# Performance work log

Hardware: AMD Instinct MI355X
Metric: run time of the kernel (lower is better)

Reference implementation:

```python
import jax, jax.numpy as jnp
import numpy as np

TOP_K = 2  # moe_top_k


def setup_inputs() -> dict:
    key = jax.random.key(0)
    k0, k1, k2, k3 = jax.random.split(key, 4)
    SL, BS, H, F, E = 2048, 4, 1024, 1024, 8
    x = jax.random.normal(k0, (SL, BS, H), dtype=jnp.float32)
    w_router = jax.random.normal(k1, (H, E), dtype=jnp.float32) * 0.02
    w1 = jax.random.normal(k2, (E, H, F), dtype=jnp.float32) * 0.02  # per-expert map weights
    w2 = jax.random.normal(k3, (E, F, H), dtype=jnp.float32) * 0.02  # per-expert reduce weights
    return {"x": x, "w_router": w_router, "w1": w1, "w2": w2}


def reference(x, w_router, w1, w2):
    # dMoA forward: router -> dropless dispatch -> per-expert map GEMM ->
    # per-expert reduce GEMM -> expert-weighted combine. Dropless = no capacity
    # dropping, so a dense all-experts compute + per-token selection is exactly
    # equivalent in math to the sort/gather/grouped-GEMM/scatter pipeline.
    sl, bs, h = x.shape
    E = w1.shape[0]
    xt = x.reshape(-1, h)  # [T, H], T = sl*bs
    T = xt.shape[0]

    # LearnedRouter: softmax over expert logits, then top-k weights/indices
    scores = jax.nn.softmax(xt @ w_router, axis=-1)       # [T, E]
    expert_weights, top_experts = jax.lax.top_k(scores, TOP_K)  # [T, K]

    # load-balancing loss (router.loss): E * sum_e f_e * p_e
    onehot = jax.nn.one_hot(top_experts, E, dtype=xt.dtype)  # [T, K, E]
    tokens_frac = onehot.sum(axis=(0, 1)) / (T * TOP_K)      # f_e
    probs_mean = scores.mean(axis=0)                         # p_e
    loss = E * jnp.sum(tokens_frac * probs_mean)

    # map: per-expert linear H->F, select the top-k experts' outputs per token
    y_all = jnp.einsum('th,ehf->tef', xt, w1)                 # [T, E, F]
    h_tk = jnp.take_along_axis(y_all, top_experts[:, :, None], axis=1)  # [T, K, F]

    # reduce: weighted scatter-combine, then per-expert linear F->H
    hw = jnp.einsum('tke,tk,tkf->tef', onehot, expert_weights, h_tk)  # [T, E, F]
    out = jnp.einsum('tef,efh->th', hw, w2)                   # [T, H]
    return out.reshape(sl, bs, h), loss
```

## Files before the change

### kernel.cpp

```cpp
#include <hip/hip_runtime.h>
#include <hip/hip_bf16.h>
#include <stdint.h>


#define HD 1024
#define FD 1024
#define EN 8

typedef __attribute__((ext_vector_type(8))) short bf16x8;
typedef __attribute__((ext_vector_type(4))) float f32x4;

__device__ __forceinline__ void gload16(const void* g, void* l) {
    __builtin_amdgcn_global_load_lds(
        (const __attribute__((address_space(1))) unsigned int*)g,
        (__attribute__((address_space(3))) unsigned int*)l, 16, 0, 0);
}

__device__ __forceinline__ ushort f2bf(float v) {
    __hip_bfloat16 h = __float2bfloat16(v);
    return *(ushort*)&h;
}
__device__ __forceinline__ float bf2f(ushort u) {
    unsigned int w = ((unsigned int)u) << 16;
    float f; __builtin_memcpy(&f, &w, 4); return f;
}

__global__ __launch_bounds__(256) void router_kernel(
    const float* __restrict__ x, const float* __restrict__ wrt,
    ushort* __restrict__ xb,
    int* __restrict__ top_e, float* __restrict__ top_w,
    int* __restrict__ counts, float* __restrict__ probsum)
{
    __shared__ int   cnt_s[EN];
    __shared__ float ps_s[EN];
    int tid = threadIdx.x;
    if (tid < EN) { cnt_s[tid] = 0; ps_s[tid] = 0.f; }
    __syncthreads();

    int wid = tid >> 6, lane = tid & 63;
    int t = blockIdx.x * 4 + wid;
    const float4* xr4 = (const float4*)(x + (size_t)t * HD);
    ushort4* xbo = (ushort4*)(xb + (size_t)t * HD);
    float acc[EN];
#pragma unroll
    for (int e = 0; e < EN; e++) acc[e] = 0.f;
#pragma unroll
    for (int it = 0; it < 4; it++) {
        float4 xv = xr4[it * 64 + lane];
        ushort4 o; o.x = f2bf(xv.x); o.y = f2bf(xv.y); o.z = f2bf(xv.z); o.w = f2bf(xv.w);
        xbo[it * 64 + lane] = o;
        int h0 = it * 256 + lane * 4;
        float xs[4] = {xv.x, xv.y, xv.z, xv.w};
#pragma unroll
        for (int j = 0; j < 4; j++) {
            const float4* wp = (const float4*)(wrt + (size_t)(h0 + j) * EN);
            float4 wa = wp[0], wb = wp[1];
            acc[0] += xs[j] * wa.x; acc[1] += xs[j] * wa.y;
            acc[2] += xs[j] * wa.z; acc[3] += xs[j] * wa.w;
            acc[4] += xs[j] * wb.x; acc[5] += xs[j] * wb.y;
            acc[6] += xs[j] * wb.z; acc[7] += xs[j] * wb.w;
        }
    }
#pragma unroll
    for (int off = 32; off >= 1; off >>= 1) {
#pragma unroll
        for (int e = 0; e < EN; e++) acc[e] += __shfl_xor(acc[e], off, 64);
    }
    if (lane == 0) {
        float m = acc[0];
#pragma unroll
        for (int e = 1; e < EN; e++) m = fmaxf(m, acc[e]);
        float p[EN], s = 0.f;
#pragma unroll
        for (int e = 0; e < EN; e++) { p[e] = expf(acc[e] - m); s += p[e]; }
        float inv = 1.f / s;
#pragma unroll
        for (int e = 0; e < EN; e++) p[e] *= inv;
        int e0 = 0;
#pragma unroll
        for (int e = 1; e < EN; e++) if (p[e] > p[e0]) e0 = e;
        int e1 = (e0 == 0) ? 1 : 0;
#pragma unroll
        for (int e = 0; e < EN; e++) {
            if (e == e0) continue;
            if (p[e] > p[e1]) e1 = e;
        }
        top_e[t * 2] = e0;  top_e[t * 2 + 1] = e1;
        top_w[t * 2] = p[e0]; top_w[t * 2 + 1] = p[e1];
        atomicAdd(&cnt_s[e0], 1); atomicAdd(&cnt_s[e1], 1);
#pragma unroll
        for (int e = 0; e < EN; e++) atomicAdd(&ps_s[e], p[e]);
    }
    __syncthreads();
    if (tid < EN) {
        atomicAdd(&counts[tid], cnt_s[tid]);
        atomicAdd(&probsum[tid], ps_s[tid]);
    }
}

__global__ void prep_kernel(const int* __restrict__ counts,
                            const float* __restrict__ probsum,
                            int* __restrict__ offs, float* __restrict__ loss_out)
{
    int off = 0; float loss = 0.f;
    for (int e = 0; e < EN; e++) {
        offs[e] = off;
        off += counts[e];
        loss += ((float)counts[e] / 16384.f) * (probsum[e] / 8192.f);
    }
    offs[EN] = off;
    *loss_out = 8.f * loss;
}

__global__ __launch_bounds__(256) void dispatch_kernel(
    const int* __restrict__ top_e, const float* __restrict__ top_w,
    const int* __restrict__ offs, int* __restrict__ cursor,
    int* __restrict__ tok_list, float* __restrict__ w_list)
{
    int t = blockIdx.x * 256 + threadIdx.x;
    int lane = threadIdx.x & 63;
#pragma unroll
    for (int k = 0; k < 2; k++) {
        int e = top_e[t * 2 + k];
        int idx = 0;
#pragma unroll
        for (int ex = 0; ex < EN; ex++) {
            unsigned long long m = __ballot(e == ex);
            if (e == ex) {
                int cnt = __popcll(m);
                int leader = __ffsll(m) - 1;
                int pos = 0;
                if (lane == leader) pos = atomicAdd(&cursor[ex * 16], cnt);
                pos = __shfl(pos, leader, 64);
                int rank = __popcll(m & ((1ull << lane) - 1ull));
                idx = offs[ex] + pos + rank;
            }
        }
        tok_list[idx] = t * 2 + k;
        w_list[idx] = top_w[t * 2 + k];
    }
}

__global__ __launch_bounds__(256) void transpose_conv_kernel(
    const float* __restrict__ w1, const float* __restrict__ w2,
    ushort* __restrict__ w1b, ushort* __restrict__ w2b)
{
    __shared__ float tile[32][33];
    int bid = blockIdx.x;
    const float* in; ushort* outp;
    if (bid >= 8192) { in = w2; outp = w2b; bid -= 8192; }
    else             { in = w1; outp = w1b; }
    int e  = bid >> 10;
    int t2 = bid & 1023;
    int tb = t2 >> 5;
    int ta = t2 & 31;
    const float* pin = in + ((size_t)e << 20);
    ushort* pout = outp + ((size_t)e << 20);
    int tx = threadIdx.x & 31, ty = threadIdx.x >> 5;
#pragma unroll
    for (int j = 0; j < 4; j++)
        tile[ty + j * 8][tx] = pin[(size_t)(ta * 32 + ty + j * 8) * 1024 + tb * 32 + tx];
    __syncthreads();
#pragma unroll
    for (int j = 0; j < 4; j++)
        pout[(size_t)(tb * 32 + ty + j * 8) * 1024 + ta * 32 + tx] =
            f2bf(tile[tx][ty + j * 8]);
}


__global__ __launch_bounds__(256) void map_gemm(
    const ushort* __restrict__ xb, const ushort* __restrict__ w1b,
    ushort* __restrict__ hbuf,
    const int* __restrict__ tok_list, const float* __restrict__ w_list,
    const int* __restrict__ offs)
{
    __shared__ __align__(16) short lA[128][64];
    __shared__ __align__(16) short lB[128][64];
    __shared__ int   tok_s[128];
    __shared__ float wt_s[128];

    int g = blockIdx.x;
    int e = g & 7, q = g >> 3, nb = q & 7, rb = q >> 3;
    int base = offs[e], cnt = offs[e + 1] - base;
    int row0 = rb << 7;
    if (row0 >= cnt) return;
    int rem = cnt - row0;
    int tid = threadIdx.x;
    if (tid < 128) {
        int r = row0 + tid; if (r > cnt - 1) r = cnt - 1;
        tok_s[tid] = tok_list[base + r];
        wt_s[tid]  = w_list[base + r];
    }
    __syncthreads();

    int lane = tid & 63, w = tid >> 6;
    int wm = w >> 1, wn = w & 1;
    int lo = lane & 15, hi = lane >> 4, rx = lane & 7;

    int lr = lane >> 3;
    int kseg = ((lane & 7) ^ lr) << 3;
    const ushort* pA[4]; const ushort* pB[4];
    const ushort* wbase = w1b + ((size_t)e << 20);
#pragma unroll
    for (int i = 0; i < 4; i++) {
        int rowT = w * 32 + i * 8 + lr;
        pA[i] = xb + (size_t)(tok_s[rowT] >> 1) * HD + kseg;
        pB[i] = wbase + (size_t)(nb * 128 + rowT) * HD + kseg;
    }

    f32x4 acc[4][4];
#pragma unroll
    for (int m = 0; m < 4; m++)
#pragma unroll
        for (int n = 0; n < 4; n++) acc[m][n] = (f32x4){0.f, 0.f, 0.f, 0.f};

    for (int kt = 0; kt < 16; ++kt) {
#pragma unroll
        for (int i = 0; i < 4; i++) {
            int rowT = w * 32 + i * 8 + lr;
            gload16(pA[i], &lA[rowT][0]);
            gload16(pB[i], &lB[rowT][0]);
            pA[i] += 64; pB[i] += 64;
        }
        __syncthreads();
        bf16x8 af[4][2], bg[4][2];
#pragma unroll
        for (int m = 0; m < 4; m++)
#pragma unroll
            for (int ks = 0; ks < 2; ks++)
                af[m][ks] = *(const bf16x8*)&lA[wm * 64 + m * 16 + lo][((ks * 4 + hi) ^ rx) << 3];
#pragma unroll
        for (int n = 0; n < 4; n++)
#pragma unroll
            for (int ks = 0; ks < 2; ks++)
                bg[n][ks] = *(const bf16x8*)&lB[wn * 64 + n * 16 + lo][((ks * 4 + hi) ^ rx) << 3];
#pragma unroll
        for (int ks = 0; ks < 2; ks++)
#pragma unroll
            for (int m = 0; m < 4; m++)
#pragma unroll
                for (int n = 0; n < 4; n++)
                    acc[m][n] = __builtin_amdgcn_mfma_f32_16x16x32_bf16(af[m][ks], bg[n][ks], acc[m][n], 0, 0, 0);
        __syncthreads();
    }

    short* ep = ((short*)lA) + w * 4096;
#pragma unroll
    for (int m = 0; m < 4; m++)
#pragma unroll
        for (int r = 0; r < 4; r++) {
            int row_l = m * 16 + hi * 4 + r;
            int rswz = (row_l & 7) << 4;
            float wgt = wt_s[wm * 64 + row_l];
#pragma unroll
            for (int n = 0; n < 4; n++) {
                int colb = (n * 16 + lo) * 2;
                ep[(row_l * 128 + (colb ^ rswz)) >> 1] = f2bf(acc[m][n][r] * wgt);
            }
        }
    __syncthreads();
    size_t outbase = (size_t)(base + row0);
    int colg0 = (nb << 7) + wn * 64;
#pragma unroll
    for (int j = 0; j < 8; j++) {
        int row_l = j * 8 + (lane >> 3);
        int r_blk = wm * 64 + row_l;
        int sb = ((lane & 7) * 16) ^ ((row_l & 7) << 4);
        bf16x8 v = *(const bf16x8*)&ep[(row_l * 128 + sb) >> 1];
        if (r_blk < rem)
            *(bf16x8*)&hbuf[(outbase + r_blk) * FD + colg0 + (lane & 7) * 8] = v;
    }
}

__global__ __launch_bounds__(256) void reduce_gemm(
    const ushort* __restrict__ hbuf, const ushort* __restrict__ w2b,
    ushort* __restrict__ obuf,
    const int* __restrict__ tok_list, const int* __restrict__ offs)
{
    __shared__ __align__(16) short lA[128][64];
    __shared__ __align__(16) short lB[128][64];
    __shared__ int tok_s[128];

    int g = blockIdx.x;
    int e = g & 7, q = g >> 3, nb = q & 7, rb = q >> 3;
    int base = offs[e], cnt = offs[e + 1] - base;
    int row0 = rb << 7;
    if (row0 >= cnt) return;
    int rem = cnt - row0;
    int tid = threadIdx.x;
    if (tid < 128) {
        int r = row0 + tid; if (r > cnt - 1) r = cnt - 1;
        tok_s[tid] = tok_list[base + r];
    }
    __syncthreads();

    int lane = tid & 63, w = tid >> 6;
    int wm = w >> 1, wn = w & 1;
    int lo = lane & 15, hi = lane >> 4, rx = lane & 7;

    int lr = lane >> 3;
    int kseg = ((lane & 7) ^ lr) << 3;
    const ushort* pA[4]; const ushort* pB[4];
    const ushort* wbase = w2b + ((size_t)e << 20);
#pragma unroll
    for (int i = 0; i < 4; i++) {
        int rowT = w * 32 + i * 8 + lr;
        int ar = row0 + rowT; if (ar > cnt - 1) ar = cnt - 1;
        pA[i] = hbuf + (size_t)(base + ar) * FD + kseg;
        pB[i] = wbase + (size_t)(nb * 128 + rowT) * FD + kseg;
    }

    f32x4 acc[4][4];
#pragma unroll
    for (int m = 0; m < 4; m++)
#pragma unroll
        for (int n = 0; n < 4; n++) acc[m][n] = (f32x4){0.f, 0.f, 0.f, 0.f};

    for (int kt = 0; kt < 16; ++kt) {
#pragma unroll
        for (int i = 0; i < 4; i++) {
            int rowT = w * 32 + i * 8 + lr;
            gload16(pA[i], &lA[rowT][0]);
            gload16(pB[i], &lB[rowT][0]);
            pA[i] += 64; pB[i] += 64;
        }
        __syncthreads();
        bf16x8 af[4][2], bg[4][2];
#pragma unroll
        for (int m = 0; m < 4; m++)
#pragma unroll
            for (int ks = 0; ks < 2; ks++)
                af[m][ks] = *(const bf16x8*)&lA[wm * 64 + m * 16 + lo][((ks * 4 + hi) ^ rx) << 3];
#pragma unroll
        for (int n = 0; n < 4; n++)
#pragma unroll
            for (int ks = 0; ks < 2; ks++)
                bg[n][ks] = *(const bf16x8*)&lB[wn * 64 + n * 16 + lo][((ks * 4 + hi) ^ rx) << 3];
#pragma unroll
        for (int ks = 0; ks < 2; ks++)
#pragma unroll
            for (int m = 0; m < 4; m++)
#pragma unroll
                for (int n = 0; n < 4; n++)
                    acc[m][n] = __builtin_amdgcn_mfma_f32_16x16x32_bf16(af[m][ks], bg[n][ks], acc[m][n], 0, 0, 0);
        __syncthreads();
    }

    short* ep = ((short*)lA) + w * 4096;
#pragma unroll
    for (int m = 0; m < 4; m++)
#pragma unroll
        for (int r = 0; r < 4; r++) {
            int row_l = m * 16 + hi * 4 + r;
            int rswz = (row_l & 7) << 4;
#pragma unroll
            for (int n = 0; n < 4; n++) {
                int colb = (n * 16 + lo) * 2;
                ep[(row_l * 128 + (colb ^ rswz)) >> 1] = f2bf(acc[m][n][r]);
            }
        }
    __syncthreads();
    int colg0 = (nb << 7) + wn * 64;
#pragma unroll
    for (int j = 0; j < 8; j++) {
        int row_l = j * 8 + (lane >> 3);
        int r_blk = wm * 64 + row_l;
        int sb = ((lane & 7) * 16) ^ ((row_l & 7) << 4);
        bf16x8 v = *(const bf16x8*)&ep[(row_l * 128 + sb) >> 1];
        if (r_blk < rem)
            *(bf16x8*)&obuf[(size_t)tok_s[r_blk] * HD + colg0 + (lane & 7) * 8] = v;
    }
}

__global__ __launch_bounds__(256) void combine_kernel(
    const ushort* __restrict__ obuf, float* __restrict__ out)
{
    int g = blockIdx.x * 256 + threadIdx.x;
    int t = g >> 7, c8 = (g & 127) << 3;
    const ushort* p = obuf + (size_t)t * 2048 + c8;
    bf16x8 a = *(const bf16x8*)p;
    bf16x8 b = *(const bf16x8*)(p + 1024);
    float o[8];
#pragma unroll
    for (int i = 0; i < 8; i++)
        o[i] = bf2f((ushort)a[i]) + bf2f((ushort)b[i]);
    float* q = out + (size_t)t * HD + c8;
    *(float4*)q       = (float4){o[0], o[1], o[2], o[3]};
    *(float4*)(q + 4) = (float4){o[4], o[5], o[6], o[7]};
}

extern "C" void kernel_launch(void* const* d_in, const int* in_sizes, int n_in,
                              void* d_out, int out_size, void* d_ws, size_t ws_size,
                              hipStream_t stream)
{
    const float* x   = (const float*)d_in[0];
    const float* wrt = (const float*)d_in[1];
    const float* w1  = (const float*)d_in[2];
    const float* w2  = (const float*)d_in[3];
    float* out = (float*)d_out;

    uint8_t* ws = (uint8_t*)d_ws;
    ushort* xb   = (ushort*)(ws);
    ushort* w1b  = (ushort*)(ws + (16u << 20));
    ushort* obuf = (ushort*)(ws);
    ushort* w2b  = (ushort*)(ws + (32u << 20));
    ushort* hbuf = (ushort*)(ws + (48u << 20));
    uint8_t* p80 = ws + (80u << 20);
    int*   tok_list = (int*)(p80);
    float* w_list   = (float*)(p80 + (64u << 10));
    int*   top_e    = (int*)(p80 + (128u << 10));
    float* top_w    = (float*)(p80 + (192u << 10));
    uint8_t* ctr    = p80 + (256u << 10);
    int*   counts   = (int*)(ctr);
    float* probsum  = (float*)(ctr + 64);
    int*   offs     = (int*)(ctr + 128);
    int*   cursor   = (int*)(ctr + 256);
    float* loss_out = out + 8388608;

    hipMemsetAsync(ctr, 0, 1024, stream);

    router_kernel<<<2048, 256, 0, stream>>>(x, wrt, xb, top_e, top_w, counts, probsum);
    prep_kernel<<<1, 1, 0, stream>>>(counts, probsum, offs, loss_out);
    dispatch_kernel<<<32, 256, 0, stream>>>(top_e, top_w, offs, cursor, tok_list, w_list);
    transpose_conv_kernel<<<16384, 256, 0, stream>>>(w1, w2, w1b, w2b);
    map_gemm<<<1152, 256, 0, stream>>>(xb, w1b, hbuf, tok_list, w_list, offs);
    reduce_gemm<<<1152, 256, 0, stream>>>(hbuf, w2b, obuf, tok_list, offs);
    combine_kernel<<<4096, 256, 0, stream>>>(obuf, out);
}
```

Measured before the change: 205.6 us.

## Fuse router with weight transpose, fold prep into dispatch, widen GEMM N-tile

Merges the router and weight transpose/convert into one launch. The transpose now uses 64x32 tiles with float4 loads and 16-byte bf16 stores. The single-thread prep kernel is folded into dispatch, where every thread recomputes the expert offsets from counts. Both expert GEMMs move from 128x128 to 128x256 output tiles, which halves the grid and reuses each A tile across twice as many columns, at the cost of more accumulator registers and LDS per block.

```diff
diff --git a/kernel.cpp b/kernel.cpp
--- a/kernel.cpp
+++ b/kernel.cpp
@@ -25,20 +25,53 @@
     float f; __builtin_memcpy(&f, &w, 4); return f;
 }
 
-__global__ __launch_bounds__(256) void router_kernel(
+__global__ __launch_bounds__(256) void fused_rt_kernel(
     const float* __restrict__ x, const float* __restrict__ wrt,
-    ushort* __restrict__ xb,
+    const float* __restrict__ w1, const float* __restrict__ w2,
+    ushort* __restrict__ xb, ushort* __restrict__ w1b, ushort* __restrict__ w2b,
     int* __restrict__ top_e, float* __restrict__ top_w,
     int* __restrict__ counts, float* __restrict__ probsum)
 {
+    __shared__ float smem[64 * 33];
+    int bid = blockIdx.x;
+    int tid = threadIdx.x;
+
+    if (bid < 8192) {
+        const float* in; ushort* outp;
+        if (bid >= 4096) { in = w2; outp = w2b; bid -= 4096; }
+        else             { in = w1; outp = w1b; }
+        int e  = bid >> 9;
+        int t2 = bid & 511;
+        int kt = t2 >> 5;
+        int nt = t2 & 31;
+        const float* pin = in + ((size_t)e << 20) + (size_t)(kt * 64) * 1024 + nt * 32;
+        ushort* pout = outp + ((size_t)e << 20) + (size_t)(nt * 32) * 1024 + kt * 64;
+#pragma unroll
+        for (int s = 0; s < 2; s++) {
+            int slot = s * 256 + tid;
+            int kk = slot >> 3, c4 = slot & 7;
+            float4 v = *(const float4*)(pin + (size_t)kk * 1024 + c4 * 4);
+            float* d = &smem[kk * 33 + c4 * 4];
+            d[0] = v.x; d[1] = v.y; d[2] = v.z; d[3] = v.w;
+        }
+        __syncthreads();
+        {
+            int n = tid >> 3, ks = (tid & 7) * 8;
+            ushort us[8];
+#pragma unroll
+            for (int i = 0; i < 8; i++) us[i] = f2bf(smem[(ks + i) * 33 + n]);
+            *(uint4*)(pout + (size_t)n * 1024 + ks) = *(uint4*)us;
+        }
+        return;
+    }
+
     __shared__ int   cnt_s[EN];
     __shared__ float ps_s[EN];
-    int tid = threadIdx.x;
     if (tid < EN) { cnt_s[tid] = 0; ps_s[tid] = 0.f; }
     __syncthreads();
 
     int wid = tid >> 6, lane = tid & 63;
-    int t = blockIdx.x * 4 + wid;
+    int t = (bid - 8192) * 4 + wid;
     const float4* xr4 = (const float4*)(x + (size_t)t * HD);
     ushort4* xbo = (ushort4*)(xb + (size_t)t * HD);
     float acc[EN];
@@ -98,25 +131,26 @@
     }
 }
 
-__global__ void prep_kernel(const int* __restrict__ counts,
-                            const float* __restrict__ probsum,
-                            int* __restrict__ offs, float* __restrict__ loss_out)
-{
-    int off = 0; float loss = 0.f;
-    for (int e = 0; e < EN; e++) {
-        offs[e] = off;
-        off += counts[e];
-        loss += ((float)counts[e] / 16384.f) * (probsum[e] / 8192.f);
-    }
-    offs[EN] = off;
-    *loss_out = 8.f * loss;
-}
-
 __global__ __launch_bounds__(256) void dispatch_kernel(
+    const int* __restrict__ counts, const float* __restrict__ probsum,
     const int* __restrict__ top_e, const float* __restrict__ top_w,
-    const int* __restrict__ offs, int* __restrict__ cursor,
-    int* __restrict__ tok_list, float* __restrict__ w_list)
-{
+    int* __restrict__ cursor, int* __restrict__ tok_list,
+    float* __restrict__ w_list, int* __restrict__ offs_g,
+    float* __restrict__ loss_out)
+{
+    int offs[EN + 1]; offs[0] = 0;
+#pragma unroll
+    for (int e = 0; e < EN; e++) offs[e + 1] = offs[e] + counts[e];
+    if (blockIdx.x == 0 && threadIdx.x == 0) {
+        float loss = 0.f;
+#pragma unroll
+        for (int e = 0; e < EN; e++) {
+            offs_g[e] = offs[e];
+            loss += ((float)counts[e] / 16384.f) * (probsum[e] / 8192.f);
+        }
+        offs_g[EN] = offs[EN];
+        *loss_out = 8.f * loss;
+    }
     int t = blockIdx.x * 256 + threadIdx.x;
     int lane = threadIdx.x & 63;
 #pragma unroll
@@ -141,32 +175,6 @@
     }
 }
 
-__global__ __launch_bounds__(256) void transpose_conv_kernel(
-    const float* __restrict__ w1, const float* __restrict__ w2,
-    ushort* __restrict__ w1b, ushort* __restrict__ w2b)
-{
-    __shared__ float tile[32][33];
-    int bid = blockIdx.x;
-    const float* in; ushort* outp;
-    if (bid >= 8192) { in = w2; outp = w2b; bid -= 8192; }
-    else             { in = w1; outp = w1b; }
-    int e  = bid >> 10;
-    int t2 = bid & 1023;
-    int tb = t2 >> 5;
-    int ta = t2 & 31;
-    const float* pin = in + ((size_t)e << 20);
-    ushort* pout = outp + ((size_t)e << 20);
-    int tx = threadIdx.x & 31, ty = threadIdx.x >> 5;
-#pragma unroll
-    for (int j = 0; j < 4; j++)
-        tile[ty + j * 8][tx] = pin[(size_t)(ta * 32 + ty + j * 8) * 1024 + tb * 32 + tx];
-    __syncthreads();
-#pragma unroll
-    for (int j = 0; j < 4; j++)
-        pout[(size_t)(tb * 32 + ty + j * 8) * 1024 + ta * 32 + tx] =
-            f2bf(tile[tx][ty + j * 8]);
-}
-
 
 __global__ __launch_bounds__(256) void map_gemm(
     const ushort* __restrict__ xb, const ushort* __restrict__ w1b,
@@ -174,13 +182,14 @@
     const int* __restrict__ tok_list, const float* __restrict__ w_list,
     const int* __restrict__ offs)
 {
-    __shared__ __align__(16) short lA[128][64];
-    __shared__ __align__(16) short lB[128][64];
+    __shared__ __align__(16) short LS[(128 + 256) * 64];
     __shared__ int   tok_s[128];
     __shared__ float wt_s[128];
+    short (*lA)[64] = (short(*)[64])LS;
+    short (*lB)[64] = (short(*)[64])(LS + 128 * 64);
 
     int g = blockIdx.x;
-    int e = g & 7, q = g >> 3, nb = q & 7, rb = q >> 3;
+    int e = g & 7, q = g >> 3, nb = q & 3, rb = q >> 2;
     int base = offs[e], cnt = offs[e + 1] - base;
     int row0 = rb << 7;
     if (row0 >= cnt) return;
@@ -199,29 +208,29 @@
 
     int lr = lane >> 3;
     int kseg = ((lane & 7) ^ lr) << 3;
-    const ushort* pA[4]; const ushort* pB[4];
+    const ushort* pA[4];
     const ushort* wbase = w1b + ((size_t)e << 20);
 #pragma unroll
-    for (int i = 0; i < 4; i++) {
-        int rowT = w * 32 + i * 8 + lr;
-        pA[i] = xb + (size_t)(tok_s[rowT] >> 1) * HD + kseg;
-        pB[i] = wbase + (size_t)(nb * 128 + rowT) * HD + kseg;
-    }
-
-    f32x4 acc[4][4];
+    for (int i = 0; i < 4; i++)
+        pA[i] = xb + (size_t)(tok_s[w * 32 + i * 8 + lr] >> 1) * HD + kseg;
+    const ushort* pB0 = wbase + (size_t)(nb * 256 + w * 64 + lr) * HD + kseg;
+
+    f32x4 acc[4][8];
 #pragma unroll
     for (int m = 0; m < 4; m++)
 #pragma unroll
-        for (int n = 0; n < 4; n++) acc[m][n] = (f32x4){0.f, 0.f, 0.f, 0.f};
+        for (int n = 0; n < 8; n++) acc[m][n] = (f32x4){0.f, 0.f, 0.f, 0.f};
 
     for (int kt = 0; kt < 16; ++kt) {
 #pragma unroll
         for (int i = 0; i < 4; i++) {
-            int rowT = w * 32 + i * 8 + lr;
-            gload16(pA[i], &lA[rowT][0]);
-            gload16(pB[i], &lB[rowT][0]);
-            pA[i] += 64; pB[i] += 64;
-        }
+            gload16(pA[i], &lA[w * 32 + i * 8][0]);
+            pA[i] += 64;
+        }
+#pragma unroll
+        for (int i = 0; i < 8; i++)
+            gload16(pB0 + (size_t)i * 8 * HD, &lB[w * 64 + i * 8][0]);
+        pB0 += 64;
         __syncthreads();
         bf16x8 af[4][2], bg[4][2];
 #pragma unroll
@@ -233,7 +242,7 @@
         for (int n = 0; n < 4; n++)
 #pragma unroll
             for (int ks = 0; ks < 2; ks++)
-                bg[n][ks] = *(const bf16x8*)&lB[wn * 64 + n * 16 + lo][((ks * 4 + hi) ^ rx) << 3];
+                bg[n][ks] = *(const bf16x8*)&lB[wn * 128 + n * 16 + lo][((ks * 4 + hi) ^ rx) << 3];
 #pragma unroll
         for (int ks = 0; ks < 2; ks++)
 #pragma unroll
@@ -241,34 +250,50 @@
 #pragma unroll
                 for (int n = 0; n < 4; n++)
                     acc[m][n] = __builtin_amdgcn_mfma_f32_16x16x32_bf16(af[m][ks], bg[n][ks], acc[m][n], 0, 0, 0);
-        __syncthreads();
-    }
-
-    short* ep = ((short*)lA) + w * 4096;
-#pragma unroll
-    for (int m = 0; m < 4; m++)
-#pragma unroll
-        for (int r = 0; r < 4; r++) {
-            int row_l = m * 16 + hi * 4 + r;
-            int rswz = (row_l & 7) << 4;
-            float wgt = wt_s[wm * 64 + row_l];
-#pragma unroll
-            for (int n = 0; n < 4; n++) {
-                int colb = (n * 16 + lo) * 2;
-                ep[(row_l * 128 + (colb ^ rswz)) >> 1] = f2bf(acc[m][n][r] * wgt);
+#pragma unroll
+        for (int n = 0; n < 4; n++)
+#pragma unroll
+            for (int ks = 0; ks < 2; ks++)
+                bg[n][ks] = *(const bf16x8*)&lB[wn * 128 + 64 + n * 16 + lo][((ks * 4 + hi) ^ rx) << 3];
+#pragma unroll
+        for (int ks = 0; ks < 2; ks++)
+#pragma unroll
+            for (int m = 0; m < 4; m++)
+#pragma unroll
+                for (int n = 0; n < 4; n++)
+                    acc[m][n + 4] = __builtin_amdgcn_mfma_f32_16x16x32_bf16(af[m][ks], bg[n][ks], acc[m][n + 4], 0, 0, 0);
+        __syncthreads();
+    }
+
+    short* ep = LS + w * 4096;
+    size_t outbase = (size_t)(base + row0);
+#pragma unroll
+    for (int half = 0; half < 2; half++) {
+#pragma unroll
+        for (int m = 0; m < 4; m++)
+#pragma unroll
+            for (int r = 0; r < 4; r++) {
+                int row_l = m * 16 + hi * 4 + r;
+                int rswz = (row_l & 7) << 4;
+                float wgt = wt_s[wm * 64 + row_l];
+#pragma unroll
+                for (int n = 0; n < 4; n++) {
+                    int colb = (n * 16 + lo) * 2;
+                    ep[(row_l * 128 + (colb ^ rswz)) >> 1] = f2bf(acc[m][half * 4 + n][r] * wgt);
+                }
             }
-        }
-    __syncthreads();
-    size_t outbase = (size_t)(base + row0);
-    int colg0 = (nb << 7) + wn * 64;
-#pragma unroll
-    for (int j = 0; j < 8; j++) {
-        int row_l = j * 8 + (lane >> 3);
-        int r_blk = wm * 64 + row_l;
-        int sb = ((lane & 7) * 16) ^ ((row_l & 7) << 4);
-        bf16x8 v = *(const bf16x8*)&ep[(row_l * 128 + sb) >> 1];
-        if (r_blk < rem)
-            *(bf16x8*)&hbuf[(outbase + r_blk) * FD + colg0 + (lane & 7) * 8] = v;
+        __syncthreads();
+        int colg0 = (nb << 8) + wn * 128 + half * 64;
+#pragma unroll
+        for (int j = 0; j < 8; j++) {
+            int row_l = j * 8 + (lane >> 3);
+            int r_blk = wm * 64 + row_l;
+            int sb = ((lane & 7) * 16) ^ ((row_l & 7) << 4);
+            bf16x8 v = *(const bf16x8*)&ep[(row_l * 128 + sb) >> 1];
+            if (r_blk < rem)
+                *(bf16x8*)&hbuf[(outbase + r_blk) * FD + colg0 + (lane & 7) * 8] = v;
+        }
+        __syncthreads();
     }
 }
 
@@ -277,12 +302,13 @@
     ushort* __restrict__ obuf,
     const int* __restrict__ tok_list, const int* __restrict__ offs)
 {
-    __shared__ __align__(16) short lA[128][64];
-    __shared__ __align__(16) short lB[128][64];
+    __shared__ __align__(16) short LS[(128 + 256) * 64];
     __shared__ int tok_s[128];
+    short (*lA)[64] = (short(*)[64])LS;
+    short (*lB)[64] = (short(*)[64])(LS + 128 * 64);
 
     int g = blockIdx.x;
-    int e = g & 7, q = g >> 3, nb = q & 7, rb = q >> 3;
+    int e = g & 7, q = g >> 3, nb = q & 3, rb = q >> 2;
     int base = offs[e], cnt = offs[e + 1] - base;
     int row0 = rb << 7;
     if (row0 >= cnt) return;
@@ -300,30 +326,31 @@
 
     int lr = lane >> 3;
     int kseg = ((lane & 7) ^ lr) << 3;
-    const ushort* pA[4]; const ushort* pB[4];
+    const ushort* pA[4];
     const ushort* wbase = w2b + ((size_t)e << 20);
 #pragma unroll
     for (int i = 0; i < 4; i++) {
-        int rowT = w * 32 + i * 8 + lr;
-        int ar = row0 + rowT; if (ar > cnt - 1) ar = cnt - 1;
+        int ar = row0 + w * 32 + i * 8 + lr; if (ar > cnt - 1) ar = cnt - 1;
         pA[i] = hbuf + (size_t)(base + ar) * FD + kseg;
-        pB[i] = wbase + (size_t)(nb * 128 + rowT) * FD + kseg;
-    }
-
-    f32x4 acc[4][4];
+    }
+    const ushort* pB0 = wbase + (size_t)(nb * 256 + w * 64 + lr) * FD + kseg;
+
+    f32x4 acc[4][8];
 #pragma unroll
     for (int m = 0; m < 4; m++)
 #pragma unroll
-        for (int n = 0; n < 4; n++) acc[m][n] = (f32x4){0.f, 0.f, 0.f, 0.f};
+        for (int n = 0; n < 8; n++) acc[m][n] = (f32x4){0.f, 0.f, 0.f, 0.f};
 
     for (int kt = 0; kt < 16; ++kt) {
 #pragma unroll
         for (int i = 0; i < 4; i++) {
-            int rowT = w * 32 + i * 8 + lr;
-            gload16(pA[i], &lA[rowT][0]);
-            gload16(pB[i], &lB[rowT][0]);
-            pA[i] += 64; pB[i] += 64;
-        }
+            gload16(pA[i], &lA[w * 32 + i * 8][0]);
+            pA[i] += 64;
+        }
+#pragma unroll
+        for (int i = 0; i < 8; i++)
+            gload16(pB0 + (size_t)i * 8 * FD, &lB[w * 64 + i * 8][0]);
+        pB0 += 64;
         __syncthreads();
         bf16x8 af[4][2], bg[4][2];
 #pragma unroll
@@ -335,7 +362,7 @@
         for (int n = 0; n < 4; n++)
 #pragma unroll
             for (int ks = 0; ks < 2; ks++)
-                bg[n][ks] = *(const bf16x8*)&lB[wn * 64 + n * 16 + lo][((ks * 4 + hi) ^ rx) << 3];
+                bg[n][ks] = *(const bf16x8*)&lB[wn * 128 + n * 16 + lo][((ks * 4 + hi) ^ rx) << 3];
 #pragma unroll
         for (int ks = 0; ks < 2; ks++)
 #pragma unroll
@@ -343,32 +370,48 @@
 #pragma unroll
                 for (int n = 0; n < 4; n++)
                     acc[m][n] = __builtin_amdgcn_mfma_f32_16x16x32_bf16(af[m][ks], bg[n][ks], acc[m][n], 0, 0, 0);
-        __syncthreads();
-    }
-
-    short* ep = ((short*)lA) + w * 4096;
-#pragma unroll
-    for (int m = 0; m < 4; m++)
-#pragma unroll
-        for (int r = 0; r < 4; r++) {
-            int row_l = m * 16 + hi * 4 + r;
-            int rswz = (row_l & 7) << 4;
-#pragma unroll
-            for (int n = 0; n < 4; n++) {
-                int colb = (n * 16 + lo) * 2;
-                ep[(row_l * 128 + (colb ^ rswz)) >> 1] = f2bf(acc[m][n][r]);
+#pragma unroll
+        for (int n = 0; n < 4; n++)
+#pragma unroll
+            for (int ks = 0; ks < 2; ks++)
+                bg[n][ks] = *(const bf16x8*)&lB[wn * 128 + 64 + n * 16 + lo][((ks * 4 + hi) ^ rx) << 3];
+#pragma unroll
+        for (int ks = 0; ks < 2; ks++)
+#pragma unroll
+            for (int m = 0; m < 4; m++)
+#pragma unroll
+                for (int n = 0; n < 4; n++)
+                    acc[m][n + 4] = __builtin_amdgcn_mfma_f32_16x16x32_bf16(af[m][ks], bg[n][ks], acc[m][n + 4], 0, 0, 0);
+        __syncthreads();
+    }
+
+    short* ep = LS + w * 4096;
+#pragma unroll
+    for (int half = 0; half < 2; half++) {
+#pragma unroll
+        for (int m = 0; m < 4; m++)
+#pragma unroll
+            for (int r = 0; r < 4; r++) {
+                int row_l = m * 16 + hi * 4 + r;
+                int rswz = (row_l & 7) << 4;
+#pragma unroll
+                for (int n = 0; n < 4; n++) {
+                    int colb = (n * 16 + lo) * 2;
+                    ep[(row_l * 128 + (colb ^ rswz)) >> 1] = f2bf(acc[m][half * 4 + n][r]);
+                }
             }
-        }
-    __syncthreads();
-    int colg0 = (nb << 7) + wn * 64;
-#pragma unroll
-    for (int j = 0; j < 8; j++) {
-        int row_l = j * 8 + (lane >> 3);
-        int r_blk = wm * 64 + row_l;
-        int sb = ((lane & 7) * 16) ^ ((row_l & 7) << 4);
-        bf16x8 v = *(const bf16x8*)&ep[(row_l * 128 + sb) >> 1];
-        if (r_blk < rem)
-            *(bf16x8*)&obuf[(size_t)tok_s[r_blk] * HD + colg0 + (lane & 7) * 8] = v;
+        __syncthreads();
+        int colg0 = (nb << 8) + wn * 128 + half * 64;
+#pragma unroll
+        for (int j = 0; j < 8; j++) {
+            int row_l = j * 8 + (lane >> 3);
+            int r_blk = wm * 64 + row_l;
+            int sb = ((lane & 7) * 16) ^ ((row_l & 7) << 4);
+            bf16x8 v = *(const bf16x8*)&ep[(row_l * 128 + sb) >> 1];
+            if (r_blk < rem)
+                *(bf16x8*)&obuf[(size_t)tok_s[r_blk] * HD + colg0 + (lane & 7) * 8] = v;
+        }
+        __syncthreads();
     }
 }
 
@@ -419,11 +462,11 @@
 
     hipMemsetAsync(ctr, 0, 1024, stream);
 
-    router_kernel<<<2048, 256, 0, stream>>>(x, wrt, xb, top_e, top_w, counts, probsum);
-    prep_kernel<<<1, 1, 0, stream>>>(counts, probsum, offs, loss_out);
-    dispatch_kernel<<<32, 256, 0, stream>>>(top_e, top_w, offs, cursor, tok_list, w_list);
-    transpose_conv_kernel<<<16384, 256, 0, stream>>>(w1, w2, w1b, w2b);
-    map_gemm<<<1152, 256, 0, stream>>>(xb, w1b, hbuf, tok_list, w_list, offs);
-    reduce_gemm<<<1152, 256, 0, stream>>>(hbuf, w2b, obuf, tok_list, offs);
+    fused_rt_kernel<<<10240, 256, 0, stream>>>(x, wrt, w1, w2, xb, w1b, w2b,
+                                               top_e, top_w, counts, probsum);
+    dispatch_kernel<<<32, 256, 0, stream>>>(counts, probsum, top_e, top_w,
+                                            cursor, tok_list, w_list, offs, loss_out);
+    map_gemm<<<640, 256, 0, stream>>>(xb, w1b, hbuf, tok_list, w_list, offs);
+    reduce_gemm<<<640, 256, 0, stream>>>(hbuf, w2b, obuf, tok_list, offs);
     combine_kernel<<<4096, 256, 0, stream>>>(obuf, out);
 }
```

After: 258.8 us. +25.9%, slower.
